# Kernel optimization log

Measured on AMD Instinct MI355X. Metric: run time of the kernel, lower is better.

The kernel has to match this reference:

```python
import jax, jax.numpy as jnp
import numpy as np
import math

B, L, Z, D, H, NL, K = 32, 64, 32, 512, 8, 8, 8192
DFF = 4 * D
HD = D // H

def _make_pe():
    pos = np.arange(L, dtype=np.float32)[:, None]
    div = np.exp(-math.log(10000.0) * np.arange(0, D, 2, dtype=np.float32) / D)
    pe = np.zeros((L, D), dtype=np.float32)
    pe[:, 0::2] = np.sin(pos * div)
    pe[:, 1::2] = np.cos(pos * div)
    return jnp.asarray(pe)

PE = _make_pe()  # (L, D) sinusoidal positional embedding, max_len = seq_len

def setup_inputs() -> dict:
    key = jax.random.key(0)
    ks = jax.random.split(key, 12)
    s = 0.02
    def rn(k, shape):
        return jax.random.normal(k, shape, jnp.float32) * s
    p = {}
    p["x"] = jax.random.normal(ks[0], (B, L, Z), jnp.float32)
    p["codebook"] = jax.random.normal(ks[1], (K, Z), jnp.float32)
    p["W_in"] = rn(ks[2], (Z, D)); p["b_in"] = jnp.zeros((D,), jnp.float32)
    p["sa_qkv_w"] = rn(ks[3], (NL, D, 3 * D)); p["sa_qkv_b"] = jnp.zeros((NL, 3 * D), jnp.float32)
    p["sa_out_w"] = rn(ks[4], (NL, D, D)); p["sa_out_b"] = jnp.zeros((NL, D), jnp.float32)
    p["ca_qkv_w"] = rn(ks[5], (NL, D, 3 * D)); p["ca_qkv_b"] = jnp.zeros((NL, 3 * D), jnp.float32)
    p["ca_out_w"] = rn(ks[6], (NL, D, D)); p["ca_out_b"] = jnp.zeros((NL, D), jnp.float32)
    p["ff1_w"] = rn(ks[7], (NL, D, DFF)); p["ff1_b"] = jnp.zeros((NL, DFF), jnp.float32)
    p["ff2_w"] = rn(ks[8], (NL, DFF, D)); p["ff2_b"] = jnp.zeros((NL, D), jnp.float32)
    p["ln1_g"] = jnp.ones((NL, D), jnp.float32); p["ln1_b"] = jnp.zeros((NL, D), jnp.float32)
    p["ln2_g"] = jnp.ones((NL, D), jnp.float32); p["ln2_b"] = jnp.zeros((NL, D), jnp.float32)
    p["ln3_g"] = jnp.ones((NL, D), jnp.float32); p["ln3_b"] = jnp.zeros((NL, D), jnp.float32)
    p["ln_g"] = jnp.ones((D,), jnp.float32); p["ln_b"] = jnp.zeros((D,), jnp.float32)
    p["W_out"] = rn(ks[9], (D, Z)); p["b_out"] = jnp.zeros((Z,), jnp.float32)
    return p

def _ln(x, g, b):
    m = x.mean(-1, keepdims=True)
    v = ((x - m) ** 2).mean(-1, keepdims=True)
    return (x - m) / jnp.sqrt(v + 1e-5) * g + b

def _mha(q_in, kv_in, qkv_w, qkv_b, out_w, out_b, key_mask):
    # q_in: (B, Lq, D), kv_in: (B, Lk, D); key_mask: (Lk,) bool or None
    q = q_in @ qkv_w[:, :D] + qkv_b[:D]
    k = kv_in @ qkv_w[:, D:2 * D] + qkv_b[D:2 * D]
    v = kv_in @ qkv_w[:, 2 * D:] + qkv_b[2 * D:]
    split = lambda t: t.reshape(t.shape[0], t.shape[1], H, HD)
    q, k, v = split(q), split(k), split(v)
    s = jnp.einsum('bqhd,bkhd->bhqk', q, k) / math.sqrt(HD)
    if key_mask is not None:
        s = jnp.where(key_mask[None, None, None, :], s, -1e9)
    a = jax.nn.softmax(s, axis=-1)
    o = jnp.einsum('bhqk,bkhd->bqhd', a, v).reshape(q_in.shape)
    return o @ out_w + out_b

def _forward(x, codebook, W_in, b_in, sa_qkv_w, sa_qkv_b, sa_out_w, sa_out_b,
             ca_qkv_w, ca_qkv_b, ca_out_w, ca_out_b, ff1_w, ff1_b, ff2_w, ff2_b,
             ln1_g, ln1_b, ln2_g, ln2_b, ln3_g, ln3_b, ln_g, ln_b, W_out, b_out):
    Bsz = x.shape[0]
    # prepend zero start token -> x_full (B, L+1, Z); context at step i = x_full[:, :i+1]
    x_full = jnp.concatenate([jnp.zeros((Bsz, 1, Z), x.dtype), x], axis=1)
    ctx_h0 = x_full[:, :L] @ W_in + b_in + PE  # padded context, fixed length L

    def step(i):
        key_mask = jnp.arange(L) <= i  # valid context positions 0..i
        # VQ nearest-neighbor quantize of the memory token x_full[:, i+1]
        mem = jnp.take(x_full, i + 1, axis=1)  # (B, Z)
        d2 = ((mem[:, None, :] - codebook[None, :, :]) ** 2).sum(-1)  # (B, K)
        q = jax.lax.stop_gradient(codebook[jnp.argmin(d2, axis=1)])  # (B, Z), detached
        mem_h = (q @ W_in + b_in)[:, None, :]  # (B, 1, D), no pos emb
        h = ctx_h0
        for l in range(NL):  # post-norm TransformerDecoderLayer, relu FFN
            sa = _mha(h, h, sa_qkv_w[l], sa_qkv_b[l], sa_out_w[l], sa_out_b[l], key_mask)
            h = _ln(h + sa, ln1_g[l], ln1_b[l])
            ca = _mha(h, mem_h, ca_qkv_w[l], ca_qkv_b[l], ca_out_w[l], ca_out_b[l], None)
            h = _ln(h + ca, ln2_g[l], ln2_b[l])
            ff = jax.nn.relu(h @ ff1_w[l] + ff1_b[l]) @ ff2_w[l] + ff2_b[l]
            h = _ln(h + ff, ln3_g[l], ln3_b[l])
        pred = _ln(h, ln_g, ln_b) @ W_out + b_out  # (B, L, Z)
        return jnp.take(pred, i, axis=1)  # last valid position (B, Z)

    preds = jax.lax.map(step, jnp.arange(L))  # (L, B, Z)
    return preds.transpose(1, 0, 2)  # (B, L, Z)

def reference(x, codebook, W_in, b_in, sa_qkv_w, sa_qkv_b, sa_out_w, sa_out_b,
              ca_qkv_w, ca_qkv_b, ca_out_w, ca_out_b, ff1_w, ff1_b, ff2_w, ff2_b,
              ln1_g, ln1_b, ln2_g, ln2_b, ln3_g, ln3_b, ln_g, ln_b, W_out, b_out):
    return _forward(x, codebook, W_in, b_in, sa_qkv_w, sa_qkv_b, sa_out_w, sa_out_b,
                    ca_qkv_w, ca_qkv_b, ca_out_w, ca_out_b, ff1_w, ff1_b, ff2_w, ff2_b,
                    ln1_g, ln1_b, ln2_g, ln2_b, ln3_g, ln3_b, ln_g, ln_b, W_out, b_out)
```

## Files before the change

kernel.cpp:

```cpp
#include <hip/hip_runtime.h>
#include <hip/hip_bf16.h>
#include <math.h>

#define DEV __device__ __forceinline__

typedef unsigned short u16;
typedef __attribute__((ext_vector_type(8))) short s8v;
typedef __attribute__((ext_vector_type(4))) float f4v;

constexpr int NLAY = 8;
constexpr int SB   = 64 * 32;
constexpr size_t RAGG = 66560;

DEV float bf2f(u16 u) { unsigned x = ((unsigned)u) << 16; union { unsigned u; float f; } c; c.u = x; return c.f; }
DEV u16 f2bf(float f) { union { float f; unsigned u; } c; c.f = f; unsigned x = c.u; x += 0x7fffu + ((x >> 16) & 1u); return (u16)(x >> 16); }

DEV void load8bf(const u16* p, float* o) {
  uint4 q = *(const uint4*)p;
  o[0] = bf2f((u16)(q.x & 0xffff)); o[1] = bf2f((u16)(q.x >> 16));
  o[2] = bf2f((u16)(q.y & 0xffff)); o[3] = bf2f((u16)(q.y >> 16));
  o[4] = bf2f((u16)(q.z & 0xffff)); o[5] = bf2f((u16)(q.z >> 16));
  o[6] = bf2f((u16)(q.w & 0xffff)); o[7] = bf2f((u16)(q.w >> 16));
}
DEV void store8bf(u16* p, const float* v) {
  uint4 q;
  q.x = (unsigned)f2bf(v[0]) | ((unsigned)f2bf(v[1]) << 16);
  q.y = (unsigned)f2bf(v[2]) | ((unsigned)f2bf(v[3]) << 16);
  q.z = (unsigned)f2bf(v[4]) | ((unsigned)f2bf(v[5]) << 16);
  q.w = (unsigned)f2bf(v[6]) | ((unsigned)f2bf(v[7]) << 16);
  *(uint4*)p = q;
}

DEV size_t seqoff(int s, int b) { return (size_t)16 * s * (s + 1) + (size_t)b * (s + 1); }

DEV void cp16(const void* g, void* l) {
  __builtin_amdgcn_global_load_lds((const __attribute__((address_space(1))) unsigned*)g,
                                   (__attribute__((address_space(3))) unsigned*)l, 16, 0, 0);
}

template<int RELU>
__global__ __launch_bounds__(256) void gemm_bt(const u16* __restrict__ A, const u16* __restrict__ Bt,
                                               const float* __restrict__ bias, u16* __restrict__ C,
                                               int N, int K) {
  __shared__ u16 As[128 * 64];
  __shared__ u16 Bs[128 * 64];
  const int tid = threadIdx.x, w = tid >> 6, lane = tid & 63;
  const int lrow = lane & 15, lquad = lane >> 4;
  const int m0 = blockIdx.y * 128, n0 = blockIdx.x * 128;
  const int wm = (w & 1) * 64, wn = (w >> 1) * 64;
  const int srow = lane >> 3, sch = (lane & 7) * 8;
  f4v acc[4][4] = {};
  for (int kt = 0; kt < K; kt += 64) {
    __syncthreads();
#pragma unroll
    for (int c = 0; c < 4; ++c) {
      int seg = w * 4 + c;
      cp16(A + (size_t)(m0 + seg * 8 + srow) * K + kt + sch, &As[seg * 512]);
      cp16(Bt + (size_t)(n0 + seg * 8 + srow) * K + kt + sch, &Bs[seg * 512]);
    }
    __syncthreads();
#pragma unroll
    for (int kc = 0; kc < 2; ++kc) {
      s8v a[4], b[4];
#pragma unroll
      for (int t = 0; t < 4; ++t) {
        a[t] = *(const s8v*)&As[(wm + t * 16 + lrow) * 64 + kc * 32 + lquad * 8];
        b[t] = *(const s8v*)&Bs[(wn + t * 16 + lrow) * 64 + kc * 32 + lquad * 8];
      }
#pragma unroll
      for (int mt = 0; mt < 4; ++mt)
#pragma unroll
        for (int nt = 0; nt < 4; ++nt)
          acc[mt][nt] = __builtin_amdgcn_mfma_f32_16x16x32_bf16(a[mt], b[nt], acc[mt][nt], 0, 0, 0);
    }
  }
#pragma unroll
  for (int nt = 0; nt < 4; ++nt) {
    int col = n0 + wn + nt * 16 + lrow;
    float bv = bias[col];
#pragma unroll
    for (int mt = 0; mt < 4; ++mt) {
      size_t rbase = (size_t)(m0 + wm + mt * 16 + lquad * 4);
#pragma unroll
      for (int j = 0; j < 4; ++j) {
        float v = acc[mt][nt][j] + bv;
        if (RELU) v = fmaxf(v, 0.f);
        C[(rbase + j) * (size_t)N + col] = f2bf(v);
      }
    }
  }
}

__global__ __launch_bounds__(256) void k_attn(const u16* __restrict__ qkv, u16* __restrict__ o,
                                              int sbase, size_t row0) {
  const int h = blockIdx.x, b = blockIdx.y, sl = blockIdx.z;
  const int s = sbase + sl;
  const size_t soff = seqoff(s, b) - row0;
  __shared__ u16 qs[64][72], ks[64][72], vts[64][72], ps[64][72];
  const int tid = threadIdx.x;
  const int row = tid >> 2, c16 = (tid & 3) * 16;
  const int rcl = row <= s ? row : s;
  {
    const u16* qp = qkv + (soff + rcl) * 1536 + h * 64 + c16;
    *(uint4*)&qs[row][c16]     = *(const uint4*)qp;
    *(uint4*)&qs[row][c16 + 8] = *(const uint4*)(qp + 8);
    *(uint4*)&ks[row][c16]     = *(const uint4*)(qp + 512);
    *(uint4*)&ks[row][c16 + 8] = *(const uint4*)(qp + 520);
    uint4 v0 = *(const uint4*)(qp + 1024), v1 = *(const uint4*)(qp + 1032);
    unsigned arr[8] = {v0.x, v0.y, v0.z, v0.w, v1.x, v1.y, v1.z, v1.w};
#pragma unroll
    for (int j = 0; j < 8; ++j) {
      vts[c16 + 2 * j][row]     = (u16)(arr[j] & 0xffff);
      vts[c16 + 2 * j + 1][row] = (u16)(arr[j] >> 16);
    }
  }
  __syncthreads();
  const int w = tid >> 6, lane = tid & 63, lrow = lane & 15, lquad = lane >> 4;
  f4v sc[4] = {};
  {
    s8v aq[2];
#pragma unroll
    for (int kc = 0; kc < 2; ++kc) aq[kc] = *(const s8v*)&qs[w * 16 + lrow][kc * 32 + lquad * 8];
#pragma unroll
    for (int nt = 0; nt < 4; ++nt)
#pragma unroll
      for (int kc = 0; kc < 2; ++kc) {
        s8v bk = *(const s8v*)&ks[nt * 16 + lrow][kc * 32 + lquad * 8];
        sc[nt] = __builtin_amdgcn_mfma_f32_16x16x32_bf16(aq[kc], bk, sc[nt], 0, 0, 0);
      }
  }
#pragma unroll
  for (int j = 0; j < 4; ++j) {
    float v[4]; float mx = -3.0e38f;
#pragma unroll
    for (int nt = 0; nt < 4; ++nt) {
      int col = nt * 16 + lrow;
      float xx = sc[nt][j] * 0.125f;
      if (col > s) xx = -1e9f;
      v[nt] = xx; mx = fmaxf(mx, xx);
    }
#pragma unroll
    for (int m = 1; m < 16; m <<= 1) mx = fmaxf(mx, __shfl_xor(mx, m));
    float sum = 0.f;
#pragma unroll
    for (int nt = 0; nt < 4; ++nt) { v[nt] = __expf(v[nt] - mx); sum += v[nt]; }
#pragma unroll
    for (int m = 1; m < 16; m <<= 1) sum += __shfl_xor(sum, m);
    float inv = 1.f / sum;
    int prow = w * 16 + lquad * 4 + j;
#pragma unroll
    for (int nt = 0; nt < 4; ++nt) ps[prow][nt * 16 + lrow] = f2bf(v[nt] * inv);
  }
  f4v oc[4] = {};
  {
    s8v ap[2];
#pragma unroll
    for (int kc = 0; kc < 2; ++kc) ap[kc] = *(const s8v*)&ps[w * 16 + lrow][kc * 32 + lquad * 8];
#pragma unroll
    for (int nt = 0; nt < 4; ++nt)
#pragma unroll
      for (int kc = 0; kc < 2; ++kc) {
        s8v bv = *(const s8v*)&vts[nt * 16 + lrow][kc * 32 + lquad * 8];
        oc[nt] = __builtin_amdgcn_mfma_f32_16x16x32_bf16(ap[kc], bv, oc[nt], 0, 0, 0);
      }
  }
#pragma unroll
  for (int nt = 0; nt < 4; ++nt) {
    int col = h * 64 + nt * 16 + lrow;
#pragma unroll
    for (int j = 0; j < 4; ++j) {
      int r = w * 16 + lquad * 4 + j;
      if (r <= s) o[(soff + r) * 512 + col] = f2bf(oc[nt][j]);
    }
  }
}

template<int HAS2>
__global__ __launch_bounds__(256) void k_ln(u16* __restrict__ hb, const u16* __restrict__ tmpb,
                                            const u16* __restrict__ cab, const int* __restrict__ map,
                                            size_t row0,
                                            const float* __restrict__ g1, const float* __restrict__ b1,
                                            const float* __restrict__ g2, const float* __restrict__ b2) {
  const int row = blockIdx.x * 4 + (threadIdx.x >> 6);
  const int lane = threadIdx.x & 63;
  const size_t off = (size_t)row * 512 + lane * 8;
  float hv[8], tv[8], t[8];
  load8bf(hb + off, hv); load8bf(tmpb + off, tv);
  float s = 0.f, ss = 0.f;
#pragma unroll
  for (int i = 0; i < 8; ++i) { t[i] = hv[i] + tv[i]; s += t[i]; ss += t[i] * t[i]; }
#pragma unroll
  for (int m = 1; m < 64; m <<= 1) { s += __shfl_xor(s, m); ss += __shfl_xor(ss, m); }
  float mean = s * (1.f / 512.f);
  float inv = 1.f / sqrtf(ss * (1.f / 512.f) - mean * mean + 1e-5f);
  float gv[8], bv[8];
  *(float4*)&gv[0] = *(const float4*)(g1 + lane * 8); *(float4*)&gv[4] = *(const float4*)(g1 + lane * 8 + 4);
  *(float4*)&bv[0] = *(const float4*)(b1 + lane * 8); *(float4*)&bv[4] = *(const float4*)(b1 + lane * 8 + 4);
  if (HAS2) {
    const int seq = map[row0 + row];
    float cv[8]; load8bf(cab + (size_t)seq * 512 + lane * 8, cv);
    float s2 = 0.f, ss2 = 0.f;
#pragma unroll
    for (int i = 0; i < 8; ++i) { float n = (t[i] - mean) * inv * gv[i] + bv[i] + cv[i]; t[i] = n; s2 += n; ss2 += n * n; }
#pragma unroll
    for (int m = 1; m < 64; m <<= 1) { s2 += __shfl_xor(s2, m); ss2 += __shfl_xor(ss2, m); }
    float mean2 = s2 * (1.f / 512.f);
    float inv2 = 1.f / sqrtf(ss2 * (1.f / 512.f) - mean2 * mean2 + 1e-5f);
    float g2v[8], b2v[8];
    *(float4*)&g2v[0] = *(const float4*)(g2 + lane * 8); *(float4*)&g2v[4] = *(const float4*)(g2 + lane * 8 + 4);
    *(float4*)&b2v[0] = *(const float4*)(b2 + lane * 8); *(float4*)&b2v[4] = *(const float4*)(b2 + lane * 8 + 4);
#pragma unroll
    for (int i = 0; i < 8; ++i) t[i] = (t[i] - mean2) * inv2 * g2v[i] + b2v[i];
  } else {
#pragma unroll
    for (int i = 0; i < 8; ++i) t[i] = (t[i] - mean) * inv * gv[i] + bv[i];
  }
  store8bf(hb + off, t);
}

__global__ __launch_bounds__(256) void k_ctx(const float* __restrict__ x, const float* __restrict__ W_in,
                                             const float* __restrict__ b_in, u16* __restrict__ ctx0) {
  const int e = blockIdx.x * 256 + threadIdx.x;
  const int d = e & 511, l = (e >> 9) & 63, b = e >> 15;
  float acc = b_in[d];
  if (l > 0) {
    const float* xr = x + (size_t)(b * 64 + l - 1) * 32;
#pragma unroll 8
    for (int z = 0; z < 32; ++z) acc += xr[z] * W_in[z * 512 + d];
  }
  const float dv = __expf(-9.210340371976184f * (float)(d & ~1) * (1.f / 512.f));
  const float ang = (float)l * dv;
  acc += (d & 1) ? cosf(ang) : sinf(ang);
  ctx0[(size_t)e] = f2bf(acc);
}

__global__ __launch_bounds__(64) void k_map(int* __restrict__ map) {
  const int seq = blockIdx.x;
  const int s = seq >> 5, b = seq & 31;
  const int l = threadIdx.x;
  if (l <= s) map[seqoff(s, b) + l] = seq;
}

__global__ __launch_bounds__(256) void k_rep(const u16* __restrict__ ctx0, u16* __restrict__ hb,
                                             int sbase, size_t row0) {
  const int sl = blockIdx.x >> 5, b = blockIdx.x & 31;
  const int s = sbase + sl;
  const size_t dst0 = seqoff(s, b) - row0;
  const int tid = threadIdx.x;
  for (int idx = tid; idx < (s + 1) * 64; idx += 256) {
    const int l = idx >> 6, d8 = idx & 63;
    *(uint4*)(hb + (dst0 + l) * 512 + d8 * 8) =
        *(const uint4*)(ctx0 + ((size_t)(b * 64 + l) * 512) + d8 * 8);
  }
}

__global__ __launch_bounds__(256) void k_vq(const float* __restrict__ x, const float* __restrict__ cb,
                                            const float* __restrict__ W_in, const float* __restrict__ b_in,
                                            u16* __restrict__ memh) {
  const int tok = blockIdx.x;
  const int s = tok >> 5, b = tok & 31;
  const int tid = threadIdx.x;
  __shared__ float xs[32], cs[32];
  __shared__ float rd[256]; __shared__ int ri[256];
  if (tid < 32) xs[tid] = x[(size_t)(b * 64 + s) * 32 + tid];
  __syncthreads();
  float bd = 3.0e38f; int bi = 0;
  for (int c = tid; c < 8192; c += 256) {
    const float4* cr = (const float4*)(cb + (size_t)c * 32);
    float d = 0.f;
#pragma unroll
    for (int z4 = 0; z4 < 8; ++z4) {
      float4 cv = cr[z4];
      float d0 = xs[z4 * 4 + 0] - cv.x, d1 = xs[z4 * 4 + 1] - cv.y;
      float d2 = xs[z4 * 4 + 2] - cv.z, d3 = xs[z4 * 4 + 3] - cv.w;
      d += d0 * d0 + d1 * d1 + d2 * d2 + d3 * d3;
    }
    if (d < bd) { bd = d; bi = c; }
  }
  rd[tid] = bd; ri[tid] = bi;
  __syncthreads();
  for (int st = 128; st > 0; st >>= 1) {
    if (tid < st) {
      float dn = rd[tid + st]; int in2 = ri[tid + st];
      if (dn < rd[tid] || (dn == rd[tid] && in2 < ri[tid])) { rd[tid] = dn; ri[tid] = in2; }
    }
    __syncthreads();
  }
  const int kmin = ri[0];
  if (tid < 32) cs[tid] = cb[(size_t)kmin * 32 + tid];
  __syncthreads();
  for (int o = tid; o < 512; o += 256) {
    float a = b_in[o];
#pragma unroll 8
    for (int z = 0; z < 32; ++z) a += cs[z] * W_in[z * 512 + o];
    memh[(size_t)tok * 512 + o] = f2bf(a);
  }
}

__global__ __launch_bounds__(64) void k_final(const u16* __restrict__ hb, const float* __restrict__ g,
                                              const float* __restrict__ bta, const float* __restrict__ Wout,
                                              const float* __restrict__ bout, float* __restrict__ out,
                                              int sbase, size_t row0) {
  const int blk = blockIdx.x;
  const int s = sbase + (blk >> 5), b = blk & 31;
  const int lane = threadIdx.x;
  __shared__ float ns[512];
  const size_t roff = (seqoff(s, b) - row0 + s) * 512;
  float v[8]; load8bf(hb + roff + lane * 8, v);
  float sm = 0.f, ssm = 0.f;
#pragma unroll
  for (int i = 0; i < 8; ++i) { sm += v[i]; ssm += v[i] * v[i]; }
#pragma unroll
  for (int m = 1; m < 64; m <<= 1) { sm += __shfl_xor(sm, m); ssm += __shfl_xor(ssm, m); }
  float mean = sm * (1.f / 512.f);
  float inv = 1.f / sqrtf(ssm * (1.f / 512.f) - mean * mean + 1e-5f);
#pragma unroll
  for (int i = 0; i < 8; ++i) ns[lane * 8 + i] = (v[i] - mean) * inv * g[lane * 8 + i] + bta[lane * 8 + i];
  __syncthreads();
  const int col = lane & 31, half = lane >> 5;
  float a = 0.f;
  for (int k = half * 256; k < half * 256 + 256; ++k) a += ns[k] * Wout[(size_t)k * 32 + col];
  a += __shfl_xor(a, 32);
  if (lane < 32) out[((size_t)b * 64 + s) * 32 + col] = a + bout[col];
}

__global__ void k_tcast(const float* __restrict__ src, u16* __restrict__ dst, int R, int C, int ld, int col0) {
  const int l = blockIdx.z;
  src += (size_t)l * R * ld;
  dst += (size_t)l * R * C;
  __shared__ float t[32][33];
  const int c0 = blockIdx.x * 32, r0 = blockIdx.y * 32;
  const int tx = threadIdx.x, ty = threadIdx.y;
#pragma unroll
  for (int k = 0; k < 4; ++k)
    t[ty + 8 * k][tx] = src[(size_t)(r0 + ty + 8 * k) * ld + col0 + c0 + tx];
  __syncthreads();
#pragma unroll
  for (int k = 0; k < 4; ++k)
    dst[(size_t)(c0 + ty + 8 * k) * R + r0 + tx] = f2bf(t[tx][ty + 8 * k]);
}

extern "C" void kernel_launch(void* const* d_in, const int* in_sizes, int n_in,
                              void* d_out, int out_size, void* d_ws, size_t ws_size,
                              hipStream_t stream) {
  (void)in_sizes; (void)n_in; (void)out_size;
  const float* x    = (const float*)d_in[0];
  const float* cb   = (const float*)d_in[1];
  const float* W_in = (const float*)d_in[2];
  const float* b_in = (const float*)d_in[3];
  const float* saqw = (const float*)d_in[4];
  const float* saqb = (const float*)d_in[5];
  const float* saow = (const float*)d_in[6];
  const float* saob = (const float*)d_in[7];
  const float* caqw = (const float*)d_in[8];
  const float* caqb = (const float*)d_in[9];
  const float* caow = (const float*)d_in[10];
  const float* caob = (const float*)d_in[11];
  const float* f1w  = (const float*)d_in[12];
  const float* f1b  = (const float*)d_in[13];
  const float* f2w  = (const float*)d_in[14];
  const float* f2b  = (const float*)d_in[15];
  const float* l1g  = (const float*)d_in[16];
  const float* l1b  = (const float*)d_in[17];
  const float* l2g  = (const float*)d_in[18];
  const float* l2b  = (const float*)d_in[19];
  const float* l3g  = (const float*)d_in[20];
  const float* l3b  = (const float*)d_in[21];
  const float* lng  = (const float*)d_in[22];
  const float* lnb  = (const float*)d_in[23];
  const float* Wout = (const float*)d_in[24];
  const float* bout = (const float*)d_in[25];
  float* out = (float*)d_out;

  u16* ws = (u16*)d_ws;
  size_t off = 0;
  auto alloc = [&](size_t n) { u16* p = ws + off; off += n; return p; };
  u16* ctx0  = alloc((size_t)32 * 64 * 512);
  u16* cabuf = alloc((size_t)NLAY * SB * 512);
  u16* memh  = alloc((size_t)SB * 512);
  u16* tmpv  = alloc((size_t)SB * 512);
  u16* wqkvT = alloc((size_t)NLAY * 1536 * 512);
  u16* woutT = alloc((size_t)NLAY * 512 * 512);
  u16* wf1T  = alloc((size_t)NLAY * 2048 * 512);
  u16* wf2T  = alloc((size_t)NLAY * 512 * 2048);
  u16* wcavT = alloc((size_t)NLAY * 512 * 512);
  u16* wcaoT = alloc((size_t)NLAY * 512 * 512);
  int* rowmap = (int*)alloc(RAGG * 2);

  size_t avail = ws_size / 2 > off ? ws_size / 2 - off : 0;
  size_t Ralloc = avail / 3072;
  Ralloc = Ralloc / 128 * 128;
  if (Ralloc > RAGG) Ralloc = RAGG;

  u16* hb   = alloc(Ralloc * 512);
  u16* regA = alloc(Ralloc * 2048);
  u16* tmpb = alloc(Ralloc * 512);
  u16* qkvb = regA;
  u16* attb = regA + Ralloc * 1536;
  u16* midb = regA;

  dim3 tb(32, 8);
  k_tcast<<<dim3(48, 16, 8), tb, 0, stream>>>(saqw, wqkvT, 512, 1536, 1536, 0);
  k_tcast<<<dim3(16, 16, 8), tb, 0, stream>>>(saow, woutT, 512, 512, 512, 0);
  k_tcast<<<dim3(64, 16, 8), tb, 0, stream>>>(f1w, wf1T, 512, 2048, 2048, 0);
  k_tcast<<<dim3(16, 64, 8), tb, 0, stream>>>(f2w, wf2T, 2048, 512, 512, 0);
  k_tcast<<<dim3(16, 16, 8), tb, 0, stream>>>(caqw, wcavT, 512, 512, 1536, 1024);
  k_tcast<<<dim3(16, 16, 8), tb, 0, stream>>>(caow, wcaoT, 512, 512, 512, 0);

  k_ctx<<<4096, 256, 0, stream>>>(x, W_in, b_in, ctx0);
  k_vq<<<2048, 256, 0, stream>>>(x, cb, W_in, b_in, memh);
  k_map<<<2048, 64, 0, stream>>>(rowmap);

  for (int l = 0; l < NLAY; ++l) {
    gemm_bt<0><<<dim3(4, 16), 256, 0, stream>>>(memh, wcavT + (size_t)l * 512 * 512,
                                                caqb + (size_t)l * 1536 + 1024, tmpv, 512, 512);
    gemm_bt<0><<<dim3(4, 16), 256, 0, stream>>>(tmpv, wcaoT + (size_t)l * 512 * 512,
                                                caob + (size_t)l * 512, cabuf + (size_t)l * SB * 512, 512, 512);
  }

  int sstart = 0;
  while (sstart < 64) {
    int send = sstart;
    size_t rows = 0;
    while (send < 64) {
      size_t nr = rows + (size_t)32 * (send + 1);
      size_t pr = (nr + 127) / 128 * 128;
      if (pr > Ralloc && send > sstart) break;
      rows = nr; ++send;
      if (pr > Ralloc) break;
    }
    const size_t row0 = (size_t)16 * sstart * (sstart + 1);
    const size_t rows_pad = (rows + 127) / 128 * 128;
    const int mg = (int)(rows_pad / 128);
    const int ns = send - sstart;

    k_rep<<<ns * 32, 256, 0, stream>>>(ctx0, hb, sstart, row0);
    for (int l = 0; l < NLAY; ++l) {
      gemm_bt<0><<<dim3(12, mg), 256, 0, stream>>>(hb, wqkvT + (size_t)l * 1536 * 512,
                                                   saqb + (size_t)l * 1536, qkvb, 1536, 512);
      k_attn<<<dim3(8, 32, ns), 256, 0, stream>>>(qkvb, attb, sstart, row0);
      gemm_bt<0><<<dim3(4, mg), 256, 0, stream>>>(attb, woutT + (size_t)l * 512 * 512,
                                                  saob + (size_t)l * 512, tmpb, 512, 512);
      k_ln<1><<<(int)(rows / 4), 256, 0, stream>>>(hb, tmpb, cabuf + (size_t)l * SB * 512,
                                                   rowmap, row0,
                                                   l1g + l * 512, l1b + l * 512, l2g + l * 512, l2b + l * 512);
      gemm_bt<1><<<dim3(16, mg), 256, 0, stream>>>(hb, wf1T + (size_t)l * 2048 * 512,
                                                   f1b + (size_t)l * 2048, midb, 2048, 512);
      gemm_bt<0><<<dim3(4, mg), 256, 0, stream>>>(midb, wf2T + (size_t)l * 512 * 2048,
                                                  f2b + (size_t)l * 512, tmpb, 512, 2048);
      k_ln<0><<<(int)(rows / 4), 256, 0, stream>>>(hb, tmpb, nullptr, rowmap, row0,
                                                   l3g + l * 512, l3b + l * 512, nullptr, nullptr);
    }
    k_final<<<ns * 32, 64, 0, stream>>>(hb, lng, lnb, Wout, bout, out, sstart, row0);
    sstart = send;
  }
}
```

Measured before the change: 8.104 ms.

## Compute only last-position rows in final decoder layer and batch cross-attn GEMMs

In the last decoder layer only the final valid position of each sequence feeds the output, so the layer now gathers those rows and runs Q projection, single-query attention, out-projection, LN and FFN on them alone. K/V are still projected for all rows. The per-layer cross-attention constant GEMMs are merged into two batched launches over a z-grid, and the VQ distance loop keeps x in registers with split accumulators. This removes most of the last layer's FFN and projection work on ragged rows, at the cost of extra small kernels and a gather.

```diff
diff --git a/kernel.cpp b/kernel.cpp
--- a/kernel.cpp
+++ b/kernel.cpp
@@ -87,6 +87,61 @@
         if (RELU) v = fmaxf(v, 0.f);
         C[(rbase + j) * (size_t)N + col] = f2bf(v);
       }
+    }
+  }
+}
+
+__global__ __launch_bounds__(256) void gemm_ca(const u16* __restrict__ A0, const u16* __restrict__ Bt0,
+                                               const float* __restrict__ bias0, u16* __restrict__ C0,
+                                               size_t sA, size_t sB, int sBias, size_t sC) {
+  const int z = blockIdx.z;
+  const u16* A = A0 + sA * z;
+  const u16* Bt = Bt0 + sB * z;
+  const float* bias = bias0 + (size_t)sBias * z;
+  u16* C = C0 + sC * z;
+  const int N = 512, K = 512;
+  __shared__ u16 As[128 * 64];
+  __shared__ u16 Bs[128 * 64];
+  const int tid = threadIdx.x, w = tid >> 6, lane = tid & 63;
+  const int lrow = lane & 15, lquad = lane >> 4;
+  const int m0 = blockIdx.y * 128, n0 = blockIdx.x * 128;
+  const int wm = (w & 1) * 64, wn = (w >> 1) * 64;
+  const int srow = lane >> 3, sch = (lane & 7) * 8;
+  f4v acc[4][4] = {};
+  for (int kt = 0; kt < K; kt += 64) {
+    __syncthreads();
+#pragma unroll
+    for (int c = 0; c < 4; ++c) {
+      int seg = w * 4 + c;
+      cp16(A + (size_t)(m0 + seg * 8 + srow) * K + kt + sch, &As[seg * 512]);
+      cp16(Bt + (size_t)(n0 + seg * 8 + srow) * K + kt + sch, &Bs[seg * 512]);
+    }
+    __syncthreads();
+#pragma unroll
+    for (int kc = 0; kc < 2; ++kc) {
+      s8v a[4], b[4];
+#pragma unroll
+      for (int t = 0; t < 4; ++t) {
+        a[t] = *(const s8v*)&As[(wm + t * 16 + lrow) * 64 + kc * 32 + lquad * 8];
+        b[t] = *(const s8v*)&Bs[(wn + t * 16 + lrow) * 64 + kc * 32 + lquad * 8];
+      }
+#pragma unroll
+      for (int mt = 0; mt < 4; ++mt)
+#pragma unroll
+        for (int nt = 0; nt < 4; ++nt)
+          acc[mt][nt] = __builtin_amdgcn_mfma_f32_16x16x32_bf16(a[mt], b[nt], acc[mt][nt], 0, 0, 0);
+    }
+  }
+#pragma unroll
+  for (int nt = 0; nt < 4; ++nt) {
+    int col = n0 + wn + nt * 16 + lrow;
+    float bv = bias[col];
+#pragma unroll
+    for (int mt = 0; mt < 4; ++mt) {
+      size_t rbase = (size_t)(m0 + wm + mt * 16 + lquad * 4);
+#pragma unroll
+      for (int j = 0; j < 4; ++j)
+        C[(rbase + j) * (size_t)N + col] = f2bf(acc[mt][nt][j] + bv);
     }
   }
 }
@@ -175,6 +230,44 @@
   }
 }
 
+__global__ __launch_bounds__(64) void k_attn_last(const u16* __restrict__ qb, const u16* __restrict__ kvb,
+                                                  u16* __restrict__ attl, int sbase, size_t row0) {
+  const int h = blockIdx.x;
+  const int r = blockIdx.y;
+  const int sl = r >> 5, b = r & 31;
+  const int s = sbase + sl;
+  const size_t soff = seqoff(s, b) - row0;
+  const int lane = threadIdx.x;
+  __shared__ float qsm[64], ps[64];
+  qsm[lane] = bf2f(qb[(size_t)r * 512 + h * 64 + lane]);
+  __syncthreads();
+  float sc = -3.0e38f;
+  if (lane <= s) {
+    const u16* kp = kvb + (soff + lane) * 1024 + h * 64;
+    float acc = 0.f;
+#pragma unroll
+    for (int d = 0; d < 64; d += 8) {
+      float kv[8]; load8bf(kp + d, kv);
+#pragma unroll
+      for (int i = 0; i < 8; ++i) acc += qsm[d + i] * kv[i];
+    }
+    sc = acc * 0.125f;
+  }
+  float mx = sc;
+#pragma unroll
+  for (int m = 1; m < 64; m <<= 1) mx = fmaxf(mx, __shfl_xor(mx, m));
+  float e = (lane <= s) ? __expf(sc - mx) : 0.f;
+  float sum = e;
+#pragma unroll
+  for (int m = 1; m < 64; m <<= 1) sum += __shfl_xor(sum, m);
+  ps[lane] = e / sum;
+  __syncthreads();
+  float acc = 0.f;
+  for (int k = 0; k <= s; ++k)
+    acc += ps[k] * bf2f(kvb[(soff + k) * 1024 + 512 + h * 64 + lane]);
+  attl[(size_t)r * 512 + h * 64 + lane] = f2bf(acc);
+}
+
 template<int HAS2>
 __global__ __launch_bounds__(256) void k_ln(u16* __restrict__ hb, const u16* __restrict__ tmpb,
                                             const u16* __restrict__ cab, const int* __restrict__ map,
@@ -218,6 +311,48 @@
   store8bf(hb + off, t);
 }
 
+template<int HAS2>
+__global__ __launch_bounds__(256) void k_ln_last(u16* __restrict__ gl, const u16* __restrict__ tmpl,
+                                                 const u16* __restrict__ cab, int sbase,
+                                                 const float* __restrict__ g1, const float* __restrict__ b1,
+                                                 const float* __restrict__ g2, const float* __restrict__ b2) {
+  const int row = blockIdx.x * 4 + (threadIdx.x >> 6);
+  const int lane = threadIdx.x & 63;
+  const size_t off = (size_t)row * 512 + lane * 8;
+  float hv[8], tv[8], t[8];
+  load8bf(gl + off, hv); load8bf(tmpl + off, tv);
+  float s = 0.f, ss = 0.f;
+#pragma unroll
+  for (int i = 0; i < 8; ++i) { t[i] = hv[i] + tv[i]; s += t[i]; ss += t[i] * t[i]; }
+#pragma unroll
+  for (int m = 1; m < 64; m <<= 1) { s += __shfl_xor(s, m); ss += __shfl_xor(ss, m); }
+  float mean = s * (1.f / 512.f);
+  float inv = 1.f / sqrtf(ss * (1.f / 512.f) - mean * mean + 1e-5f);
+  float gv[8], bv[8];
+  *(float4*)&gv[0] = *(const float4*)(g1 + lane * 8); *(float4*)&gv[4] = *(const float4*)(g1 + lane * 8 + 4);
+  *(float4*)&bv[0] = *(const float4*)(b1 + lane * 8); *(float4*)&bv[4] = *(const float4*)(b1 + lane * 8 + 4);
+  if (HAS2) {
+    const int seq = (sbase + (row >> 5)) * 32 + (row & 31);
+    float cv[8]; load8bf(cab + (size_t)seq * 512 + lane * 8, cv);
+    float s2 = 0.f, ss2 = 0.f;
+#pragma unroll
+    for (int i = 0; i < 8; ++i) { float n = (t[i] - mean) * inv * gv[i] + bv[i] + cv[i]; t[i] = n; s2 += n; ss2 += n * n; }
+#pragma unroll
+    for (int m = 1; m < 64; m <<= 1) { s2 += __shfl_xor(s2, m); ss2 += __shfl_xor(ss2, m); }
+    float mean2 = s2 * (1.f / 512.f);
+    float inv2 = 1.f / sqrtf(ss2 * (1.f / 512.f) - mean2 * mean2 + 1e-5f);
+    float g2v[8], b2v[8];
+    *(float4*)&g2v[0] = *(const float4*)(g2 + lane * 8); *(float4*)&g2v[4] = *(const float4*)(g2 + lane * 8 + 4);
+    *(float4*)&b2v[0] = *(const float4*)(b2 + lane * 8); *(float4*)&b2v[4] = *(const float4*)(b2 + lane * 8 + 4);
+#pragma unroll
+    for (int i = 0; i < 8; ++i) t[i] = (t[i] - mean2) * inv2 * g2v[i] + b2v[i];
+  } else {
+#pragma unroll
+    for (int i = 0; i < 8; ++i) t[i] = (t[i] - mean) * inv * gv[i] + bv[i];
+  }
+  store8bf(gl + off, t);
+}
+
 __global__ __launch_bounds__(256) void k_ctx(const float* __restrict__ x, const float* __restrict__ W_in,
                                              const float* __restrict__ b_in, u16* __restrict__ ctx0) {
   const int e = blockIdx.x * 256 + threadIdx.x;
@@ -254,6 +389,14 @@
   }
 }
 
+__global__ __launch_bounds__(64) void k_gather(const u16* __restrict__ hb, u16* __restrict__ gl,
+                                               int sbase, size_t row0) {
+  const int r = blockIdx.x; const int sl = r >> 5, b = r & 31; const int s = sbase + sl;
+  const size_t src = (seqoff(s, b) - row0 + s) * 512;
+  const int lane = threadIdx.x;
+  *(uint4*)(gl + (size_t)r * 512 + lane * 8) = *(const uint4*)(hb + src + lane * 8);
+}
+
 __global__ __launch_bounds__(256) void k_vq(const float* __restrict__ x, const float* __restrict__ cb,
                                             const float* __restrict__ W_in, const float* __restrict__ b_in,
                                             u16* __restrict__ memh) {
@@ -264,17 +407,22 @@
   __shared__ float rd[256]; __shared__ int ri[256];
   if (tid < 32) xs[tid] = x[(size_t)(b * 64 + s) * 32 + tid];
   __syncthreads();
+  float xr[32];
+#pragma unroll
+  for (int i = 0; i < 32; ++i) xr[i] = xs[i];
   float bd = 3.0e38f; int bi = 0;
+#pragma unroll 2
   for (int c = tid; c < 8192; c += 256) {
     const float4* cr = (const float4*)(cb + (size_t)c * 32);
-    float d = 0.f;
+    float d0 = 0.f, d1 = 0.f, d2 = 0.f, d3 = 0.f;
 #pragma unroll
     for (int z4 = 0; z4 < 8; ++z4) {
       float4 cv = cr[z4];
-      float d0 = xs[z4 * 4 + 0] - cv.x, d1 = xs[z4 * 4 + 1] - cv.y;
-      float d2 = xs[z4 * 4 + 2] - cv.z, d3 = xs[z4 * 4 + 3] - cv.w;
-      d += d0 * d0 + d1 * d1 + d2 * d2 + d3 * d3;
-    }
+      float t0 = xr[z4 * 4 + 0] - cv.x, t1 = xr[z4 * 4 + 1] - cv.y;
+      float t2 = xr[z4 * 4 + 2] - cv.z, t3 = xr[z4 * 4 + 3] - cv.w;
+      d0 += t0 * t0; d1 += t1 * t1; d2 += t2 * t2; d3 += t3 * t3;
+    }
+    float d = (d0 + d1) + (d2 + d3);
     if (d < bd) { bd = d; bi = c; }
   }
   rd[tid] = bd; ri[tid] = bi;
@@ -297,16 +445,16 @@
   }
 }
 
-__global__ __launch_bounds__(64) void k_final(const u16* __restrict__ hb, const float* __restrict__ g,
+__global__ __launch_bounds__(64) void k_final(const u16* __restrict__ gl, const float* __restrict__ g,
                                               const float* __restrict__ bta, const float* __restrict__ Wout,
                                               const float* __restrict__ bout, float* __restrict__ out,
-                                              int sbase, size_t row0) {
+                                              int sbase) {
   const int blk = blockIdx.x;
   const int s = sbase + (blk >> 5), b = blk & 31;
   const int lane = threadIdx.x;
   __shared__ float ns[512];
-  const size_t roff = (seqoff(s, b) - row0 + s) * 512;
-  float v[8]; load8bf(hb + roff + lane * 8, v);
+  const size_t roff = (size_t)blk * 512;
+  float v[8]; load8bf(gl + roff + lane * 8, v);
   float sm = 0.f, ssm = 0.f;
 #pragma unroll
   for (int i = 0; i < 8; ++i) { sm += v[i]; ssm += v[i] * v[i]; }
@@ -378,7 +526,7 @@
   u16* ctx0  = alloc((size_t)32 * 64 * 512);
   u16* cabuf = alloc((size_t)NLAY * SB * 512);
   u16* memh  = alloc((size_t)SB * 512);
-  u16* tmpv  = alloc((size_t)SB * 512);
+  u16* tmpv8 = alloc((size_t)NLAY * SB * 512);
   u16* wqkvT = alloc((size_t)NLAY * 1536 * 512);
   u16* woutT = alloc((size_t)NLAY * 512 * 512);
   u16* wf1T  = alloc((size_t)NLAY * 2048 * 512);
@@ -387,6 +535,12 @@
   u16* wcaoT = alloc((size_t)NLAY * 512 * 512);
   int* rowmap = (int*)alloc(RAGG * 2);
 
+  u16* glast = tmpv8;
+  u16* qb    = tmpv8 + 1048576;
+  u16* attl  = tmpv8 + 2 * 1048576;
+  u16* tmpl  = tmpv8 + 3 * 1048576;
+  u16* midl  = tmpv8 + 4 * 1048576;
+
   size_t avail = ws_size / 2 > off ? ws_size / 2 - off : 0;
   size_t Ralloc = avail / 3072;
   Ralloc = Ralloc / 128 * 128;
@@ -398,6 +552,7 @@
   u16* qkvb = regA;
   u16* attb = regA + Ralloc * 1536;
   u16* midb = regA;
+  u16* kvb  = regA;
 
   dim3 tb(32, 8);
   k_tcast<<<dim3(48, 16, 8), tb, 0, stream>>>(saqw, wqkvT, 512, 1536, 1536, 0);
@@ -411,12 +566,10 @@
   k_vq<<<2048, 256, 0, stream>>>(x, cb, W_in, b_in, memh);
   k_map<<<2048, 64, 0, stream>>>(rowmap);
 
-  for (int l = 0; l < NLAY; ++l) {
-    gemm_bt<0><<<dim3(4, 16), 256, 0, stream>>>(memh, wcavT + (size_t)l * 512 * 512,
-                                                caqb + (size_t)l * 1536 + 1024, tmpv, 512, 512);
-    gemm_bt<0><<<dim3(4, 16), 256, 0, stream>>>(tmpv, wcaoT + (size_t)l * 512 * 512,
-                                                caob + (size_t)l * 512, cabuf + (size_t)l * SB * 512, 512, 512);
-  }
+  gemm_ca<<<dim3(4, 16, 8), 256, 0, stream>>>(memh, wcavT, caqb + 1024, tmpv8,
+                                              0, (size_t)512 * 512, 1536, (size_t)SB * 512);
+  gemm_ca<<<dim3(4, 16, 8), 256, 0, stream>>>(tmpv8, wcaoT, caob, cabuf,
+                                              (size_t)SB * 512, (size_t)512 * 512, 512, (size_t)SB * 512);
 
   int sstart = 0;
   while (sstart < 64) {
@@ -433,9 +586,11 @@
     const size_t rows_pad = (rows + 127) / 128 * 128;
     const int mg = (int)(rows_pad / 128);
     const int ns = send - sstart;
-
-    k_rep<<<ns * 32, 256, 0, stream>>>(ctx0, hb, sstart, row0);
-    for (int l = 0; l < NLAY; ++l) {
+    const int nseq = ns * 32;
+    const int nseqp = (nseq + 127) / 128 * 128;
+
+    k_rep<<<nseq, 256, 0, stream>>>(ctx0, hb, sstart, row0);
+    for (int l = 0; l < NLAY - 1; ++l) {
       gemm_bt<0><<<dim3(12, mg), 256, 0, stream>>>(hb, wqkvT + (size_t)l * 1536 * 512,
                                                    saqb + (size_t)l * 1536, qkvb, 1536, 512);
       k_attn<<<dim3(8, 32, ns), 256, 0, stream>>>(qkvb, attb, sstart, row0);
@@ -451,7 +606,26 @@
       k_ln<0><<<(int)(rows / 4), 256, 0, stream>>>(hb, tmpb, nullptr, rowmap, row0,
                                                    l3g + l * 512, l3b + l * 512, nullptr, nullptr);
     }
-    k_final<<<ns * 32, 64, 0, stream>>>(hb, lng, lnb, Wout, bout, out, sstart, row0);
+    {
+      const size_t l7q = (size_t)7 * 1536 * 512;
+      k_gather<<<nseq, 64, 0, stream>>>(hb, glast, sstart, row0);
+      gemm_bt<0><<<dim3(8, mg), 256, 0, stream>>>(hb, wqkvT + l7q + (size_t)512 * 512,
+                                                  saqb + 7 * 1536 + 512, kvb, 1024, 512);
+      gemm_bt<0><<<dim3(4, nseqp / 128), 256, 0, stream>>>(glast, wqkvT + l7q,
+                                                           saqb + 7 * 1536, qb, 512, 512);
+      k_attn_last<<<dim3(8, nseq), 64, 0, stream>>>(qb, kvb, attl, sstart, row0);
+      gemm_bt<0><<<dim3(4, nseqp / 128), 256, 0, stream>>>(attl, woutT + (size_t)7 * 512 * 512,
+                                                           saob + 7 * 512, tmpl, 512, 512);
+      k_ln_last<1><<<nseq / 4, 256, 0, stream>>>(glast, tmpl, cabuf + (size_t)7 * SB * 512, sstart,
+                                                 l1g + 7 * 512, l1b + 7 * 512, l2g + 7 * 512, l2b + 7 * 512);
+      gemm_bt<1><<<dim3(16, nseqp / 128), 256, 0, stream>>>(glast, wf1T + (size_t)7 * 2048 * 512,
+                                                            f1b + (size_t)7 * 2048, midl, 2048, 512);
+      gemm_bt<0><<<dim3(4, nseqp / 128), 256, 0, stream>>>(midl, wf2T + (size_t)7 * 512 * 2048,
+                                                           f2b + 7 * 512, tmpl, 512, 2048);
+      k_ln_last<0><<<nseq / 4, 256, 0, stream>>>(glast, tmpl, nullptr, sstart,
+                                                 l3g + 7 * 512, l3b + 7 * 512, nullptr, nullptr);
+      k_final<<<nseq, 64, 0, stream>>>(glast, lng, lnb, Wout, bout, out, sstart);
+    }
     sstart = send;
   }
 }
```

Result: faster. 7.550 ms (-6.8%).
